# Kernel optimization log

Hardware: AMD Instinct MI355X
Metric: run time of the kernel (lower is better)

The kernel has to match this reference:

```python
import jax, jax.numpy as jnp
import numpy as np

HEADS = 4
KS = 7       # kernel size
PAD = 3      # same padding for stride 1


def conv1x1(x, W, b):
    # x: (B,C,H,W), W: (O,C), b: (O,)
    return jnp.einsum('oc,bchw->bohw', W, x) + b[None, :, None, None]


def unfold(x):
    # im2col: (B, C*KS*KS, H, W) with channel-major ordering (C, kh, kw), matching torch.nn.Unfold
    B, C, H, W = x.shape
    p = jax.lax.conv_general_dilated_patches(
        x, filter_shape=(KS, KS), window_strides=(1, 1),
        padding=((PAD, PAD), (PAD, PAD)))
    mid = C // HEADS
    return p.reshape(B, HEADS, mid, KS * KS, H, W)


def setup_inputs() -> dict:
    key = jax.random.key(0)
    ks = jax.random.split(key, 7)
    C = 64
    scale = 1.0 / np.sqrt(C)
    x = jax.random.normal(ks[0], (4, C, 128, 128), dtype=jnp.float32)
    Wq = jax.random.normal(ks[1], (C, C), dtype=jnp.float32) * scale
    bq = jax.random.normal(ks[2], (C,), dtype=jnp.float32) * 0.01
    Wk = jax.random.normal(ks[3], (C, C), dtype=jnp.float32) * scale
    bk = jax.random.normal(ks[4], (C,), dtype=jnp.float32) * 0.01
    Wv = jax.random.normal(ks[5], (C, C), dtype=jnp.float32) * scale
    bv = jax.random.normal(ks[6], (C,), dtype=jnp.float32) * 0.01
    return {"x": x, "Wq": Wq, "bq": bq, "Wk": Wk, "bk": bk, "Wv": Wv, "bv": bv}


def reference(x, Wq, bq, Wk, bk, Wv, bv):
    B, C, H, W = x.shape
    mid = C // HEADS
    Q = conv1x1(x, Wq, bq).reshape(B, HEADS, mid, H, W)
    K = unfold(conv1x1(x, Wk, bk))  # (B,g,c,P,H,W)
    V = unfold(conv1x1(x, Wv, bv))  # (B,g,c,P,H,W)
    A = jnp.einsum('bgchw,bgcphw->bgphw', Q, K)
    A = jax.nn.softmax(A, axis=2)
    y = jnp.einsum('bgphw,bgcphw->bgchw', A, V).reshape(B, C, H, W)
    return x + y  # residual: in_channels == out_channels
```

## Files before the change

### kernel.cpp

```cpp
#include <hip/hip_runtime.h>

#define NB 4
#define NC 64
#define MID 16
#define NH 4
#define KS 7
#define PAD 3
#define HH 128
#define WW 128
#define TILE 16
#define HALO (TILE + KS - 1)
#define NCELL (HALO * HALO)
#define PLANE (HH * WW)

__global__ __launch_bounds__(256) void qkv_kernel(
    const float* __restrict__ x,
    const float* __restrict__ Wq, const float* __restrict__ bq,
    const float* __restrict__ Wk, const float* __restrict__ bk,
    const float* __restrict__ Wv, const float* __restrict__ bv,
    float* __restrict__ Qm, float* __restrict__ Km, float* __restrict__ Vm)
{
    __shared__ float wt[NC][68];
    __shared__ float xt[2][16][256];
    __shared__ float bias_s[NC];

    const int t = threadIdx.x;
    const int m = blockIdx.y;
    const float* Wm = (m == 0) ? Wq : (m == 1) ? Wk : Wv;
    const float* bm = (m == 0) ? bq : (m == 1) ? bk : bv;
    float*       Om = (m == 0) ? Qm : (m == 1) ? Km : Vm;

    const int tile = blockIdx.x;
    const int b    = tile >> 6;
    const int hw0  = (tile & 63) << 8;
    const float* xb = x + ((size_t)b * NC) * PLANE + hw0;

    #pragma unroll
    for (int r = 0; r < 16; ++r) {
        const int idx = (r << 8) + t;
        wt[idx & 63][idx >> 6] = Wm[idx];
    }
    if (t < NC) bias_s[t] = bm[t];

    #pragma unroll
    for (int r = 0; r < 4; ++r) {
        const int idx = (r << 8) + t;
        ((float4*)&xt[0][idx >> 6][0])[idx & 63] =
            ((const float4*)(xb + (size_t)(idx >> 6) * PLANE))[idx & 63];
    }
    __syncthreads();

    const int o0 = (t >> 5) << 3;
    const int p0 = t & 31;
    float acc[8][8];
    #pragma unroll
    for (int i = 0; i < 8; ++i)
        #pragma unroll
        for (int j = 0; j < 8; ++j) acc[i][j] = 0.f;

    for (int ck = 0; ck < 4; ++ck) {
        const int buf = ck & 1;
        float4 pre[4];
        if (ck < 3) {
            #pragma unroll
            for (int r = 0; r < 4; ++r) {
                const int idx = (r << 8) + t;
                pre[r] = ((const float4*)(xb + (size_t)((ck + 1) * 16 + (idx >> 6)) * PLANE))[idx & 63];
            }
        }
        #pragma unroll
        for (int kk = 0; kk < 16; ++kk) {
            const int c = (ck << 4) + kk;
            const float4 wa = *(const float4*)&wt[c][o0];
            const float4 wb = *(const float4*)&wt[c][o0 + 4];
            const float w8[8] = {wa.x, wa.y, wa.z, wa.w, wb.x, wb.y, wb.z, wb.w};
            float x8[8];
            #pragma unroll
            for (int j = 0; j < 8; ++j) x8[j] = xt[buf][kk][p0 + (j << 5)];
            #pragma unroll
            for (int i = 0; i < 8; ++i)
                #pragma unroll
                for (int j = 0; j < 8; ++j)
                    acc[i][j] = fmaf(w8[i], x8[j], acc[i][j]);
        }
        if (ck < 3) {
            #pragma unroll
            for (int r = 0; r < 4; ++r) {
                const int idx = (r << 8) + t;
                ((float4*)&xt[buf ^ 1][idx >> 6][0])[idx & 63] = pre[r];
            }
        }
        __syncthreads();
    }

    float* ob = Om + ((size_t)b * NC) * PLANE + hw0;
    #pragma unroll
    for (int i = 0; i < 8; ++i) {
        const float bi = bias_s[o0 + i];
        #pragma unroll
        for (int j = 0; j < 8; ++j)
            ob[(size_t)(o0 + i) * PLANE + p0 + (j << 5)] = acc[i][j] + bi;
    }
}

__global__ __launch_bounds__(256) void attn_kernel(
    const float* __restrict__ x,
    const float* __restrict__ Qm, const float* __restrict__ Km,
    const float* __restrict__ Vm, float* __restrict__ out)
{
    __shared__ float Kt[NCELL * MID];
    __shared__ float Vt[NCELL * MID];

    int blk = blockIdx.x;
    const int tx0 = (blk & 7) * TILE; blk >>= 3;
    const int ty0 = (blk & 7) * TILE; blk >>= 3;
    const int g   = blk & 3;
    const int b   = blk >> 2;

    const int t  = threadIdx.x;
    const int tx = t & 15, ty = t >> 4;

    const float* Kb = Km + ((size_t)b * NC + g * MID) * PLANE;
    const float* Vb = Vm + ((size_t)b * NC + g * MID) * PLANE;

    const size_t pbase = ((size_t)b * NC + g * MID) * PLANE
                       + (size_t)(ty0 + ty) * WW + (tx0 + tx);

    float q[MID];
    #pragma unroll
    for (int c = 0; c < MID; ++c) q[c] = Qm[pbase + c * PLANE];

    auto stage = [&](const float* base, float* T) {
        for (int i = t; i < NCELL * 4; i += 256) {
            const int cell = i >> 2;
            const int u    = i & 3;
            const int yy = cell / HALO, xx = cell - yy * HALO;
            const int h = ty0 + yy - PAD, w = tx0 + xx - PAD;
            float4 v = make_float4(0.f, 0.f, 0.f, 0.f);
            if ((h >= 0) & (h < HH) & (w >= 0) & (w < WW)) {
                const float* src = base + (size_t)(u * 4) * PLANE + h * WW + w;
                v.x = src[0];
                v.y = src[PLANE];
                v.z = src[2 * PLANE];
                v.w = src[3 * PLANE];
            }
            *(float4*)&T[(cell << 4) + ((u ^ ((cell >> 1) & 3)) << 2)] = v;
        }
    };
    stage(Kb, Kt);
    stage(Vb, Vt);
    __syncthreads();

    float l = 0.f;
    float acc[MID];
    #pragma unroll
    for (int c = 0; c < MID; ++c) acc[c] = 0.f;

    for (int kh = 0; kh < KS; ++kh) {
        const int rowc = (ty + kh) * HALO + tx;
        #pragma unroll
        for (int kw = 0; kw < KS; ++kw) {
            const int cell = rowc + kw;
            const int cb = cell << 4;
            const int sw = (cell >> 1) & 3;
            float s0 = 0.f, s1 = 0.f, s2 = 0.f, s3 = 0.f;
            {
                const float4 k0 = *(const float4*)&Kt[cb + ((0 ^ sw) << 2)];
                const float4 k1 = *(const float4*)&Kt[cb + ((1 ^ sw) << 2)];
                const float4 k2 = *(const float4*)&Kt[cb + ((2 ^ sw) << 2)];
                const float4 k3 = *(const float4*)&Kt[cb + ((3 ^ sw) << 2)];
                s0 = fmaf(q[0],  k0.x, fmaf(q[1],  k0.y, fmaf(q[2],  k0.z, q[3]  * k0.w)));
                s1 = fmaf(q[4],  k1.x, fmaf(q[5],  k1.y, fmaf(q[6],  k1.z, q[7]  * k1.w)));
                s2 = fmaf(q[8],  k2.x, fmaf(q[9],  k2.y, fmaf(q[10], k2.z, q[11] * k2.w)));
                s3 = fmaf(q[12], k3.x, fmaf(q[13], k3.y, fmaf(q[14], k3.z, q[15] * k3.w)));
            }
            const float e = __expf((s0 + s1) + (s2 + s3));
            l += e;
            #pragma unroll
            for (int u = 0; u < 4; ++u) {
                const float4 v4 = *(const float4*)&Vt[cb + ((u ^ sw) << 2)];
                acc[4 * u + 0] = fmaf(e, v4.x, acc[4 * u + 0]);
                acc[4 * u + 1] = fmaf(e, v4.y, acc[4 * u + 1]);
                acc[4 * u + 2] = fmaf(e, v4.z, acc[4 * u + 2]);
                acc[4 * u + 3] = fmaf(e, v4.w, acc[4 * u + 3]);
            }
        }
    }

    const float inv = 1.f / l;
    #pragma unroll
    for (int c = 0; c < MID; ++c) {
        const size_t idx = pbase + c * PLANE;
        out[idx] = x[idx] + acc[c] * inv;
    }
}

extern "C" void kernel_launch(void* const* d_in, const int* in_sizes, int n_in,
                              void* d_out, int out_size, void* d_ws, size_t ws_size,
                              hipStream_t stream) {
    const float* x  = (const float*)d_in[0];
    const float* Wq = (const float*)d_in[1];
    const float* bq = (const float*)d_in[2];
    const float* Wk = (const float*)d_in[3];
    const float* bk = (const float*)d_in[4];
    const float* Wv = (const float*)d_in[5];
    const float* bv = (const float*)d_in[6];
    float* out = (float*)d_out;

    const size_t map_elems = (size_t)NB * NC * PLANE;
    float* Qm = (float*)d_ws;
    float* Km = Qm + map_elems;
    float* Vm = Km + map_elems;

    dim3 g1(256, 3);
    qkv_kernel<<<g1, 256, 0, stream>>>(x, Wq, bq, Wk, bk, Wv, bv, Qm, Km, Vm);

    const int nblk = NB * NH * (HH / TILE) * (WW / TILE);
    attn_kernel<<<nblk, 256, 0, stream>>>(x, Qm, Km, Vm, out);
}
```

Before: 169.2 us.

## Store K/V tiles in fp16 LDS with fdot2 scores and vectorize qkv smem/stores

The attention kernel now converts K and V halo tiles to fp16 in shared memory, which halves LDS footprint and read bandwidth. Q·K scores are computed with packed fp16 dot2 instructions and fp32 accumulation. The qkv GEMM changes its pixel mapping so each thread reads x from shared memory and writes outputs as float4 vectors. The cost is reduced precision in the attention logits and values, plus the removal of the XOR swizzle, which may add LDS bank conflicts.

```diff
diff --git a/kernel.cpp b/kernel.cpp
--- a/kernel.cpp
+++ b/kernel.cpp
@@ -13,6 +13,24 @@
 #define NCELL (HALO * HALO)
 #define PLANE (HH * WW)
 
+typedef _Float16 h2 __attribute__((ext_vector_type(2)));
+typedef _Float16 h4 __attribute__((ext_vector_type(4)));
+typedef _Float16 h8 __attribute__((ext_vector_type(8)));
+
+__device__ __forceinline__ h2 pack2(float x, float y) {
+    h2 r; r[0] = (_Float16)x; r[1] = (_Float16)y; return r;
+}
+
+#if __has_builtin(__builtin_amdgcn_fdot2)
+#define FDOT2(a, b, c) __builtin_amdgcn_fdot2((a), (b), (c), false)
+#else
+__device__ __forceinline__ float FDOT2(h2 a, h2 b, float c) {
+    return fmaf((float)a[0], (float)b[0], fmaf((float)a[1], (float)b[1], c));
+}
+#endif
+
+#define H2OF(v, j) __builtin_shufflevector((v), (v), 2*(j), 2*(j)+1)
+
 __global__ __launch_bounds__(256) void qkv_kernel(
     const float* __restrict__ x,
     const float* __restrict__ Wq, const float* __restrict__ bq,
@@ -50,8 +68,8 @@
     }
     __syncthreads();
 
-    const int o0 = (t >> 5) << 3;
-    const int p0 = t & 31;
+    const int o0  = (t >> 5) << 3;
+    const int q04 = (t & 31) << 2;
     float acc[8][8];
     #pragma unroll
     for (int i = 0; i < 8; ++i)
@@ -74,9 +92,9 @@
             const float4 wa = *(const float4*)&wt[c][o0];
             const float4 wb = *(const float4*)&wt[c][o0 + 4];
             const float w8[8] = {wa.x, wa.y, wa.z, wa.w, wb.x, wb.y, wb.z, wb.w};
-            float x8[8];
-            #pragma unroll
-            for (int j = 0; j < 8; ++j) x8[j] = xt[buf][kk][p0 + (j << 5)];
+            const float4 xa = *(const float4*)&xt[buf][kk][q04];
+            const float4 xc = *(const float4*)&xt[buf][kk][q04 + 128];
+            const float x8[8] = {xa.x, xa.y, xa.z, xa.w, xc.x, xc.y, xc.z, xc.w};
             #pragma unroll
             for (int i = 0; i < 8; ++i)
                 #pragma unroll
@@ -97,9 +115,11 @@
     #pragma unroll
     for (int i = 0; i < 8; ++i) {
         const float bi = bias_s[o0 + i];
-        #pragma unroll
-        for (int j = 0; j < 8; ++j)
-            ob[(size_t)(o0 + i) * PLANE + p0 + (j << 5)] = acc[i][j] + bi;
+        float* orow = ob + (size_t)(o0 + i) * PLANE;
+        float4 s0 = {acc[i][0] + bi, acc[i][1] + bi, acc[i][2] + bi, acc[i][3] + bi};
+        float4 s1 = {acc[i][4] + bi, acc[i][5] + bi, acc[i][6] + bi, acc[i][7] + bi};
+        *(float4*)&orow[q04]       = s0;
+        *(float4*)&orow[q04 + 128] = s1;
     }
 }
 
@@ -108,8 +128,8 @@
     const float* __restrict__ Qm, const float* __restrict__ Km,
     const float* __restrict__ Vm, float* __restrict__ out)
 {
-    __shared__ float Kt[NCELL * MID];
-    __shared__ float Vt[NCELL * MID];
+    __shared__ _Float16 Kt[NCELL * 16];
+    __shared__ _Float16 Vt[NCELL * 16];
 
     int blk = blockIdx.x;
     const int tx0 = (blk & 7) * TILE; blk >>= 3;
@@ -126,11 +146,12 @@
     const size_t pbase = ((size_t)b * NC + g * MID) * PLANE
                        + (size_t)(ty0 + ty) * WW + (tx0 + tx);
 
-    float q[MID];
-    #pragma unroll
-    for (int c = 0; c < MID; ++c) q[c] = Qm[pbase + c * PLANE];
-
-    auto stage = [&](const float* base, float* T) {
+    h2 qh[8];
+    #pragma unroll
+    for (int c = 0; c < 8; ++c)
+        qh[c] = pack2(Qm[pbase + (2 * c) * PLANE], Qm[pbase + (2 * c + 1) * PLANE]);
+
+    auto stage = [&](const float* base, _Float16* T) {
         for (int i = t; i < NCELL * 4; i += 256) {
             const int cell = i >> 2;
             const int u    = i & 3;
@@ -144,7 +165,10 @@
                 v.z = src[2 * PLANE];
                 v.w = src[3 * PLANE];
             }
-            *(float4*)&T[(cell << 4) + ((u ^ ((cell >> 1) & 3)) << 2)] = v;
+            h4 hv;
+            hv[0] = (_Float16)v.x; hv[1] = (_Float16)v.y;
+            hv[2] = (_Float16)v.z; hv[3] = (_Float16)v.w;
+            *(h4*)&T[(cell << 4) + (u << 2)] = hv;
         }
     };
     stage(Kb, Kt);
@@ -160,30 +184,27 @@
         const int rowc = (ty + kh) * HALO + tx;
         #pragma unroll
         for (int kw = 0; kw < KS; ++kw) {
-            const int cell = rowc + kw;
-            const int cb = cell << 4;
-            const int sw = (cell >> 1) & 3;
-            float s0 = 0.f, s1 = 0.f, s2 = 0.f, s3 = 0.f;
-            {
-                const float4 k0 = *(const float4*)&Kt[cb + ((0 ^ sw) << 2)];
-                const float4 k1 = *(const float4*)&Kt[cb + ((1 ^ sw) << 2)];
-                const float4 k2 = *(const float4*)&Kt[cb + ((2 ^ sw) << 2)];
-                const float4 k3 = *(const float4*)&Kt[cb + ((3 ^ sw) << 2)];
-                s0 = fmaf(q[0],  k0.x, fmaf(q[1],  k0.y, fmaf(q[2],  k0.z, q[3]  * k0.w)));
-                s1 = fmaf(q[4],  k1.x, fmaf(q[5],  k1.y, fmaf(q[6],  k1.z, q[7]  * k1.w)));
-                s2 = fmaf(q[8],  k2.x, fmaf(q[9],  k2.y, fmaf(q[10], k2.z, q[11] * k2.w)));
-                s3 = fmaf(q[12], k3.x, fmaf(q[13], k3.y, fmaf(q[14], k3.z, q[15] * k3.w)));
-            }
-            const float e = __expf((s0 + s1) + (s2 + s3));
+            const int cb = (rowc + kw) << 4;
+            const h8 k0 = *(const h8*)&Kt[cb];
+            const h8 k1 = *(const h8*)&Kt[cb + 8];
+            float sa = FDOT2(H2OF(k0, 0), qh[0], 0.f);
+            float sb = FDOT2(H2OF(k1, 0), qh[4], 0.f);
+            sa = FDOT2(H2OF(k0, 1), qh[1], sa);
+            sb = FDOT2(H2OF(k1, 1), qh[5], sb);
+            sa = FDOT2(H2OF(k0, 2), qh[2], sa);
+            sb = FDOT2(H2OF(k1, 2), qh[6], sb);
+            sa = FDOT2(H2OF(k0, 3), qh[3], sa);
+            sb = FDOT2(H2OF(k1, 3), qh[7], sb);
+            const float e = __expf(sa + sb);
             l += e;
-            #pragma unroll
-            for (int u = 0; u < 4; ++u) {
-                const float4 v4 = *(const float4*)&Vt[cb + ((u ^ sw) << 2)];
-                acc[4 * u + 0] = fmaf(e, v4.x, acc[4 * u + 0]);
-                acc[4 * u + 1] = fmaf(e, v4.y, acc[4 * u + 1]);
-                acc[4 * u + 2] = fmaf(e, v4.z, acc[4 * u + 2]);
-                acc[4 * u + 3] = fmaf(e, v4.w, acc[4 * u + 3]);
-            }
+            const h8 v0 = *(const h8*)&Vt[cb];
+            const h8 v1 = *(const h8*)&Vt[cb + 8];
+            #pragma unroll
+            for (int j = 0; j < 8; ++j)
+                acc[j] = fmaf(e, (float)v0[j], acc[j]);
+            #pragma unroll
+            for (int j = 0; j < 8; ++j)
+                acc[8 + j] = fmaf(e, (float)v1[j], acc[8 + j]);
         }
     }
 
```

New measurement: 158.9 us. -6.1%, faster.
